# Performance work log

Measured on AMD Instinct MI355X. Metric: run time of the kernel, lower is better.

Reference implementation:

```python
import jax, jax.numpy as jnp
import numpy as np

HID = 128
DEPTH = 3
N_TREE = 6000
N_GRAPH = 144000
N = N_TREE + N_GRAPH
E = 600000
B = 4096
ATOM_FDIM = 34
EPS = 1e-8


def expmap0(u):
    # Lorentz expmap at origin (k=1); u has zero time component u[:,0]=0
    sp = u[:, 1:]
    nrm = jnp.clip(jnp.sqrt(jnp.sum(sp * sp, axis=-1, keepdims=True)), EPS)
    return jnp.concatenate([jnp.cosh(nrm), jnp.sinh(nrm) * sp / nrm], axis=-1)


def lorentz_linear(x, W, b, scale, nonlin=None):
    # HyboNet LorentzLinear: Euclidean linear then reproject onto hyperboloid
    if nonlin is not None:
        x = nonlin(x)
    y = x @ W.T + b
    time = jax.nn.sigmoid(y[:, :1]) * jnp.exp(scale) + 1.1  # [N,1]
    rest = y[:, 1:]
    s = (time * time - 1.0) / jnp.clip(jnp.sum(rest * rest, axis=-1, keepdims=True), EPS)
    return jnp.concatenate([time, rest * jnp.sqrt(s)], axis=-1)


def centroid_denom(x):
    # sqrt(| -<x,x>_L |) = sqrt(| x0^2 - sum(rest^2) |), clamped
    d = x[:, :1] ** 2 - jnp.sum(x[:, 1:] ** 2, axis=-1, keepdims=True)
    return jnp.sqrt(jnp.clip(jnp.abs(d), EPS))


def reference(graph_features, tree_features, edge_w, W0, b0, scale0, Wl, bl, scalel,
              edge_src, edge_dst, seg_ids):
    # prepend zero time coord + expmap0 (Lorentz branch)
    gf = jnp.concatenate([jnp.zeros_like(graph_features[:, :1]), graph_features], axis=1)
    gf = expmap0(gf)
    gf = lorentz_linear(gf, W0, b0, scale0)          # [N_GRAPH, HID]
    x = jnp.concatenate([tree_features, gf], axis=0)  # [N, HID]

    # LorentzGraphConvolution layers: LorentzLinear (relu inside for i>0) + sparse agg
    h = x
    for i in range(DEPTH):
        nonlin = None if i == 0 else jax.nn.relu
        h = lorentz_linear(h, Wl[i], bl[i], scalel[i], nonlin=nonlin)
        msg = edge_w[:, None] * h[edge_src]                         # [E, HID]
        support = jax.ops.segment_sum(msg, edge_dst, num_segments=N)
        h = support / centroid_denom(support)

    # per-scope Lorentz mid-point over graph-atom rows
    hg = h[N_TREE:]
    sums = jax.ops.segment_sum(hg, seg_ids, num_segments=B)
    cnt = jax.ops.segment_sum(jnp.ones((N_GRAPH, 1), h.dtype), seg_ids, num_segments=B)
    ave = sums / jnp.clip(cnt, 1.0)
    mol_vecs = ave / centroid_denom(ave)
    return mol_vecs


def setup_inputs() -> dict:
    key = jax.random.key(0)
    ks = jax.random.split(key, 10)
    log_scale = float(np.log(10.0))
    return {
        'graph_features': jax.random.uniform(ks[0], (N_GRAPH, ATOM_FDIM), jnp.float32),
        'tree_features': jax.random.normal(ks[1], (N_TREE, HID), jnp.float32),
        'edge_w': jax.random.uniform(ks[2], (E,), jnp.float32),
        'W0': jax.random.normal(ks[3], (HID, ATOM_FDIM + 1), jnp.float32) * 0.1,
        'b0': jnp.zeros((HID,), jnp.float32),
        'scale0': jnp.full((1,), log_scale, jnp.float32),
        'Wl': jax.random.normal(ks[4], (DEPTH, HID, HID), jnp.float32) * 0.1,
        'bl': jnp.zeros((DEPTH, HID), jnp.float32),
        'scalel': jnp.full((DEPTH,), log_scale, jnp.float32),
        'edge_src': jax.random.randint(ks[5], (E,), 0, N, jnp.int32),
        'edge_dst': jax.random.randint(ks[6], (E,), 0, N, jnp.int32),
        'seg_ids': jnp.sort(jax.random.randint(ks[7], (N_GRAPH,), 0, B, jnp.int32)),
    }
```

## Files before the change

kernel.cpp:

```cpp
#include <hip/hip_runtime.h>
#include <math.h>

#define HID    128
#define NTREE  6000
#define NGRAPH 144000
#define NNODE  150000
#define NEDGE  600000
#define NSEG   4096
#define AF     34
#define EPSF   1e-8f

#define SCAN_BLK   256
#define SCAN_ELEMS 1024
#define NSCAN ((NNODE + SCAN_ELEMS - 1) / SCAN_ELEMS)


__device__ __forceinline__ float waveReduceSum(float v) {
#pragma unroll
  for (int o = 32; o > 0; o >>= 1) v += __shfl_down(v, o, 64);
  return v;
}

__device__ __forceinline__ float blockReduce128(float v, float* red) {
  v = waveReduceSum(v);
  int w = threadIdx.x >> 6;
  if ((threadIdx.x & 63) == 0) red[w] = v;
  __syncthreads();
  float r = red[0] + red[1];
  __syncthreads();
  return r;
}


__global__ void k_hist(const int* __restrict__ dst, int* __restrict__ deg) {
  int e = blockIdx.x * blockDim.x + threadIdx.x;
  if (e < NEDGE) atomicAdd(&deg[dst[e]], 1);
}

__global__ void k_scan1(const int* __restrict__ deg, int* __restrict__ off,
                        int* __restrict__ part) {
  __shared__ int s[SCAN_BLK];
  int b = blockIdx.x, t = threadIdx.x;
  int base = b * SCAN_ELEMS + t * 4;
  int v0 = 0, v1 = 0, v2 = 0, v3 = 0;
  if (base + 0 < NNODE) v0 = deg[base + 0];
  if (base + 1 < NNODE) v1 = deg[base + 1];
  if (base + 2 < NNODE) v2 = deg[base + 2];
  if (base + 3 < NNODE) v3 = deg[base + 3];
  int sum = v0 + v1 + v2 + v3;
  s[t] = sum;
  __syncthreads();
  for (int o = 1; o < SCAN_BLK; o <<= 1) {
    int x = (t >= o) ? s[t - o] : 0;
    __syncthreads();
    s[t] += x;
    __syncthreads();
  }
  int run = s[t] - sum;
  run += v0; if (base + 0 < NNODE) off[base + 1] = run;
  run += v1; if (base + 1 < NNODE) off[base + 2] = run;
  run += v2; if (base + 2 < NNODE) off[base + 3] = run;
  run += v3; if (base + 3 < NNODE) off[base + 4] = run;
  if (t == SCAN_BLK - 1) part[b] = s[t];
  if (b == 0 && t == 0) off[0] = 0;
}

__global__ void k_scan2(int* part, int nb) {
  __shared__ int s[SCAN_BLK];
  int t = threadIdx.x;
  s[t] = (t < nb) ? part[t] : 0;
  __syncthreads();
  for (int o = 1; o < SCAN_BLK; o <<= 1) {
    int x = (t >= o) ? s[t - o] : 0;
    __syncthreads();
    s[t] += x;
    __syncthreads();
  }
  if (t < nb) part[t] = s[t];
}

__global__ void k_scan3(int* __restrict__ off, const int* __restrict__ part) {
  int b = blockIdx.x;
  if (b == 0) return;
  int add = part[b - 1];
  int base = b * SCAN_ELEMS + threadIdx.x * 4 + 1;
#pragma unroll
  for (int j = 0; j < 4; j++) {
    int idx = base + j;
    if (idx <= NNODE) off[idx] += add;
  }
}

__global__ void k_fill(const int* __restrict__ dst, const int* __restrict__ src,
                       const float* __restrict__ ew, int* __restrict__ cur,
                       int* __restrict__ sperm, float* __restrict__ wperm) {
  int e = blockIdx.x * blockDim.x + threadIdx.x;
  if (e < NEDGE) {
    int d = dst[e];
    int p = atomicAdd(&cur[d], 1);
    sperm[p] = src[e];
    wperm[p] = ew[e];
  }
}


__global__ __launch_bounds__(256) void k_embed(const float* __restrict__ gfeat,
                                               const float* __restrict__ W0,
                                               const float* __restrict__ b0,
                                               const float* __restrict__ scale0,
                                               float* __restrict__ xout) {
  const int lane = threadIdx.x & 63;
  const int gwave = blockIdx.x * (blockDim.x >> 6) + (threadIdx.x >> 6);
  const int nwaves = gridDim.x * (blockDim.x >> 6);

  float wa[AF + 1], wb[AF + 1];
  {
    const float* ra = W0 + (size_t)lane * (AF + 1);
    const float* rb = W0 + (size_t)(lane + 64) * (AF + 1);
#pragma unroll
    for (int k = 0; k < AF + 1; ++k) { wa[k] = ra[k]; wb[k] = rb[k]; }
  }
  const float ba = b0[lane];
  const float bbv = b0[lane + 64];
  const float escale = expf(scale0[0]);

  for (int g = gwave; g < NGRAPH; g += nwaves) {
    float sv = (lane < AF) ? gfeat[(size_t)g * AF + lane] : 0.f;
    float ss = sv * sv;
#pragma unroll
    for (int m = 1; m <= 32; m <<= 1) ss += __shfl_xor(ss, m, 64);
    float nrm = fmaxf(sqrtf(ss), EPSF);
    float e = expf(nrm);
    float ei = 1.f / e;
    float coshv = 0.5f * (e + ei);
    float sh = 0.5f * (e - ei) / nrm;
    float gs = sh * sv;

    float acc0 = fmaf(wa[0], coshv, ba);
    float acc1 = fmaf(wb[0], coshv, bbv);
#pragma unroll
    for (int k = 1; k < AF + 1; ++k) {
      float gk = __int_as_float(
          __builtin_amdgcn_readlane(__float_as_int(gs), k - 1));
      acc0 = fmaf(wa[k], gk, acc0);
      acc1 = fmaf(wb[k], gk, acc1);
    }
    float part = ((lane == 0) ? 0.f : acc0 * acc0) + acc1 * acc1;
#pragma unroll
    for (int m = 1; m <= 32; m <<= 1) part += __shfl_xor(part, m, 64);
    float y0 = __int_as_float(__builtin_amdgcn_readlane(__float_as_int(acc0), 0));
    float timec = 1.f / (1.f + expf(-y0)) * escale + 1.1f;
    float s = (timec * timec - 1.f) / fmaxf(part, EPSF);
    float sq = sqrtf(s);
    float* orow = xout + (size_t)(NTREE + g) * HID;
    orow[lane] = (lane == 0) ? timec : acc0 * sq;
    orow[lane + 64] = acc1 * sq;
  }
}


template <int RELU>
__global__ __launch_bounds__(256) void k_linear(const float* __restrict__ in,
                                                const float* __restrict__ W,
                                                const float* __restrict__ b,
                                                const float* __restrict__ scale,
                                                float* __restrict__ out) {
  __shared__ __align__(16) float xs[32 * 32];
  __shared__ __align__(16) float wl[128 * 32];

  const int tid = threadIdx.x;
  const int tc = tid & 31;
  const int rg = tid >> 5;
  const int c0 = tc * 4;
  const int r0 = rg * 4;
  const int row_base = blockIdx.x * 32;
  const int swz = tc & 7;

  float acc[4][4];
#pragma unroll
  for (int r = 0; r < 4; r++)
#pragma unroll
    for (int c = 0; c < 4; c++) acc[r][c] = 0.f;

  const int sr  = tid >> 3;
  const int skx = (tid & 7) * 4;
  const int wcol = tid >> 1;
  const int wq0  = (tid & 1) * 4;
  const int wswz = (wcol >> 2) & 7;

  for (int kc = 0; kc < 4; ++kc) {
    __syncthreads();
    {
      int row = row_base + sr;
      float4 v = make_float4(0.f, 0.f, 0.f, 0.f);
      if (row < NNODE) v = *(const float4*)&in[(size_t)row * HID + kc * 32 + skx];
      if (RELU) {
        v.x = fmaxf(v.x, 0.f); v.y = fmaxf(v.y, 0.f);
        v.z = fmaxf(v.z, 0.f); v.w = fmaxf(v.w, 0.f);
      }
      *(float4*)&xs[sr * 32 + skx] = v;
    }
    {
      const float* wsrc = W + (size_t)wcol * HID + kc * 32 + wq0 * 4;
#pragma unroll
      for (int q = 0; q < 4; ++q) {
        float4 v = *(const float4*)&wsrc[q * 4];
        int k4 = wq0 + q;
        *(float4*)&wl[wcol * 32 + ((k4 ^ wswz) << 2)] = v;
      }
    }
    __syncthreads();
#pragma unroll
    for (int k4 = 0; k4 < 8; ++k4) {
      float4 xv[4];
      float4 wv[4];
#pragma unroll
      for (int r = 0; r < 4; ++r)
        xv[r] = *(const float4*)&xs[(r0 + r) * 32 + k4 * 4];
#pragma unroll
      for (int c = 0; c < 4; ++c)
        wv[c] = *(const float4*)&wl[(c0 + c) * 32 + ((k4 ^ swz) << 2)];
#pragma unroll
      for (int r = 0; r < 4; ++r)
#pragma unroll
        for (int c = 0; c < 4; ++c)
          acc[r][c] += wv[c].x * xv[r].x + wv[c].y * xv[r].y +
                       wv[c].z * xv[r].z + wv[c].w * xv[r].w;
    }
  }

  const float escale = expf(scale[0]);
  const float4 bb = *(const float4*)&b[c0];
#pragma unroll
  for (int r = 0; r < 4; ++r) {
    float y0v = acc[r][0] + bb.x;
    float y1v = acc[r][1] + bb.y;
    float y2v = acc[r][2] + bb.z;
    float y3v = acc[r][3] + bb.w;
    float part = y0v * y0v + y1v * y1v + y2v * y2v + y3v * y3v;
#pragma unroll
    for (int m = 1; m <= 16; m <<= 1) part += __shfl_xor(part, m, 64);
    float y0 = __shfl(y0v, (threadIdx.x & 32), 64);
    float timec = 1.f / (1.f + expf(-y0)) * escale + 1.1f;
    float ssum = part - y0 * y0;
    float s = (timec * timec - 1.f) / fmaxf(ssum, EPSF);
    float sq = sqrtf(s);
    int row = row_base + r0 + r;
    if (row < NNODE) {
      float4 o;
      o.x = (tc == 0) ? timec : y0v * sq;
      o.y = y1v * sq;
      o.z = y2v * sq;
      o.w = y3v * sq;
      *(float4*)&out[(size_t)row * HID + c0] = o;
    }
  }
}


__global__ void k_gather(const float* __restrict__ h, const int* __restrict__ off,
                         const int* __restrict__ sperm, const float* __restrict__ wperm,
                         float* __restrict__ out) {
  __shared__ float red[2];
  int n = blockIdx.x;
  int t = threadIdx.x;
  int e0 = off[n], e1 = off[n + 1];
  float acc = 0.f;
  for (int e = e0; e < e1; ++e) {
    int s = sperm[e];
    float w = wperm[e];
    acc += w * h[(size_t)s * HID + t];
  }
  float part = (t == 0) ? acc * acc : -acc * acc;
  float d = blockReduce128(part, red);
  float denom = sqrtf(fmaxf(fabsf(d), EPSF));
  out[(size_t)n * HID + t] = acc / denom;
}


__device__ __forceinline__ int lowerBound(const int* __restrict__ a, int n, int key) {
  int lo = 0, hi = n;
  while (lo < hi) {
    int mid = (lo + hi) >> 1;
    if (a[mid] < key) lo = mid + 1; else hi = mid;
  }
  return lo;
}

__global__ void k_final(const float* __restrict__ h, const int* __restrict__ seg,
                        float* __restrict__ out) {
  __shared__ float red[2];
  int bseg = blockIdx.x;
  int t = threadIdx.x;
  int lo = lowerBound(seg, NGRAPH, bseg);
  int hi = lowerBound(seg, NGRAPH, bseg + 1);
  float acc = 0.f;
  for (int r = lo; r < hi; ++r) acc += h[(size_t)(NTREE + r) * HID + t];
  float cnt = (float)(hi - lo);
  float ave = acc / fmaxf(cnt, 1.f);
  float part = (t == 0) ? ave * ave : -ave * ave;
  float d = blockReduce128(part, red);
  float denom = sqrtf(fmaxf(fabsf(d), EPSF));
  out[bseg * HID + t] = ave / denom;
}


extern "C" void kernel_launch(void* const* d_in, const int* in_sizes, int n_in,
                              void* d_out, int out_size, void* d_ws, size_t ws_size,
                              hipStream_t stream) {
  const float* gfeat  = (const float*)d_in[0];
  const float* tfeat  = (const float*)d_in[1];
  const float* ew     = (const float*)d_in[2];
  const float* W0     = (const float*)d_in[3];
  const float* b0     = (const float*)d_in[4];
  const float* scale0 = (const float*)d_in[5];
  const float* Wl     = (const float*)d_in[6];
  const float* bl     = (const float*)d_in[7];
  const float* scalel = (const float*)d_in[8];
  const int* esrc     = (const int*)d_in[9];
  const int* edst     = (const int*)d_in[10];
  const int* segids   = (const int*)d_in[11];
  float* outp = (float*)d_out;

  char* ws = (char*)d_ws;
  size_t o = 0;
  auto take = [&](size_t bytes) -> char* {
    char* p = ws + o;
    o = (o + bytes + 255) & ~(size_t)255;
    return p;
  };
  int*   off   = (int*)take((NNODE + 1) * sizeof(int));
  int*   cur   = (int*)take(NNODE * sizeof(int));
  int*   sperm = (int*)take(NEDGE * sizeof(int));
  float* wperm = (float*)take(NEDGE * sizeof(float));
  int*   part  = (int*)take(SCAN_BLK * sizeof(int));
  float* bufA  = (float*)take((size_t)NNODE * HID * sizeof(float));
  float* bufB  = (float*)take((size_t)NNODE * HID * sizeof(float));
  (void)ws_size; (void)in_sizes; (void)n_in; (void)out_size;

  hipMemsetAsync(cur, 0, NNODE * sizeof(int), stream);
  k_hist<<<(NEDGE + 255) / 256, 256, 0, stream>>>(edst, cur);
  k_scan1<<<NSCAN, SCAN_BLK, 0, stream>>>(cur, off, part);
  k_scan2<<<1, SCAN_BLK, 0, stream>>>(part, NSCAN);
  k_scan3<<<NSCAN, SCAN_BLK, 0, stream>>>(off, part);
  hipMemcpyAsync(cur, off, NNODE * sizeof(int), hipMemcpyDeviceToDevice, stream);
  k_fill<<<(NEDGE + 255) / 256, 256, 0, stream>>>(edst, esrc, ew, cur, sperm, wperm);

  hipMemcpyAsync(bufA, tfeat, (size_t)NTREE * HID * sizeof(float),
                 hipMemcpyDeviceToDevice, stream);
  k_embed<<<1024, 256, 0, stream>>>(gfeat, W0, b0, scale0, bufA);

  for (int i = 0; i < 3; i++) {
    const float* Wi = Wl + (size_t)i * HID * HID;
    const float* bi = bl + (size_t)i * HID;
    const float* si = scalel + i;
    if (i == 0)
      k_linear<0><<<(NNODE + 31) / 32, 256, 0, stream>>>(bufA, Wi, bi, si, bufB);
    else
      k_linear<1><<<(NNODE + 31) / 32, 256, 0, stream>>>(bufA, Wi, bi, si, bufB);
    k_gather<<<NNODE, 128, 0, stream>>>(bufB, off, sperm, wperm, bufA);
  }

  k_final<<<NSEG, 128, 0, stream>>>(bufA, segids, outp);
}
```

Measured before the change: 949.7 us.

## Rewrite k_linear as register-resident weights with one wave per row

Replaces the LDS-tiled 32-row GEMM with a persistent grid-stride kernel. Each lane keeps two full weight rows (256 floats) in registers, and each wave computes one output row with uniform broadcast loads of the input row. This removes shared-memory staging and barriers, but it uses very high register pressure, which lowers occupancy and may cause spills. Each row's input is read as a scalar/uniform broadcast, and arithmetic intensity per wave is lower than with the tiled kernel.

```diff
diff --git a/kernel.cpp b/kernel.cpp
--- a/kernel.cpp
+++ b/kernel.cpp
@@ -165,95 +165,64 @@
                                                 const float* __restrict__ b,
                                                 const float* __restrict__ scale,
                                                 float* __restrict__ out) {
-  __shared__ __align__(16) float xs[32 * 32];
-  __shared__ __align__(16) float wl[128 * 32];
-
-  const int tid = threadIdx.x;
-  const int tc = tid & 31;
-  const int rg = tid >> 5;
-  const int c0 = tc * 4;
-  const int r0 = rg * 4;
-  const int row_base = blockIdx.x * 32;
-  const int swz = tc & 7;
-
-  float acc[4][4];
-#pragma unroll
-  for (int r = 0; r < 4; r++)
-#pragma unroll
-    for (int c = 0; c < 4; c++) acc[r][c] = 0.f;
-
-  const int sr  = tid >> 3;
-  const int skx = (tid & 7) * 4;
-  const int wcol = tid >> 1;
-  const int wq0  = (tid & 1) * 4;
-  const int wswz = (wcol >> 2) & 7;
-
-  for (int kc = 0; kc < 4; ++kc) {
-    __syncthreads();
-    {
-      int row = row_base + sr;
-      float4 v = make_float4(0.f, 0.f, 0.f, 0.f);
-      if (row < NNODE) v = *(const float4*)&in[(size_t)row * HID + kc * 32 + skx];
+  const int lane = threadIdx.x & 63;
+  const int wv = (blockIdx.x * blockDim.x + threadIdx.x) >> 6;
+  const int nw = (gridDim.x * blockDim.x) >> 6;
+
+  float4 wa[32], wb[32];
+  {
+    const float4* ra = (const float4*)(W + (size_t)lane * HID);
+    const float4* rb = (const float4*)(W + (size_t)(lane + 64) * HID);
+#pragma unroll
+    for (int j = 0; j < 32; ++j) { wa[j] = ra[j]; wb[j] = rb[j]; }
+  }
+  const float ba = b[lane];
+  const float bbv = b[lane + 64];
+  const float escale = expf(scale[0]);
+
+  for (int row = wv; row < NNODE; row += nw) {
+    const int urow = __builtin_amdgcn_readfirstlane(row);
+    const float* xr = in + (size_t)urow * HID;
+    float a0 = 0.f, a1 = 0.f, a2 = 0.f, a3 = 0.f;
+#pragma unroll
+    for (int j = 0; j < 32; j += 2) {
+      float4 x0 = *(const float4*)&xr[j * 4];
+      float4 x1 = *(const float4*)&xr[j * 4 + 4];
       if (RELU) {
-        v.x = fmaxf(v.x, 0.f); v.y = fmaxf(v.y, 0.f);
-        v.z = fmaxf(v.z, 0.f); v.w = fmaxf(v.w, 0.f);
+        x0.x = fmaxf(x0.x, 0.f); x0.y = fmaxf(x0.y, 0.f);
+        x0.z = fmaxf(x0.z, 0.f); x0.w = fmaxf(x0.w, 0.f);
+        x1.x = fmaxf(x1.x, 0.f); x1.y = fmaxf(x1.y, 0.f);
+        x1.z = fmaxf(x1.z, 0.f); x1.w = fmaxf(x1.w, 0.f);
       }
-      *(float4*)&xs[sr * 32 + skx] = v;
+      a0 = fmaf(wa[j].x, x0.x, a0);
+      a2 = fmaf(wb[j].x, x0.x, a2);
+      a1 = fmaf(wa[j + 1].x, x1.x, a1);
+      a3 = fmaf(wb[j + 1].x, x1.x, a3);
+      a0 = fmaf(wa[j].y, x0.y, a0);
+      a2 = fmaf(wb[j].y, x0.y, a2);
+      a1 = fmaf(wa[j + 1].y, x1.y, a1);
+      a3 = fmaf(wb[j + 1].y, x1.y, a3);
+      a0 = fmaf(wa[j].z, x0.z, a0);
+      a2 = fmaf(wb[j].z, x0.z, a2);
+      a1 = fmaf(wa[j + 1].z, x1.z, a1);
+      a3 = fmaf(wb[j + 1].z, x1.z, a3);
+      a0 = fmaf(wa[j].w, x0.w, a0);
+      a2 = fmaf(wb[j].w, x0.w, a2);
+      a1 = fmaf(wa[j + 1].w, x1.w, a1);
+      a3 = fmaf(wb[j + 1].w, x1.w, a3);
     }
-    {
-      const float* wsrc = W + (size_t)wcol * HID + kc * 32 + wq0 * 4;
-#pragma unroll
-      for (int q = 0; q < 4; ++q) {
-        float4 v = *(const float4*)&wsrc[q * 4];
-        int k4 = wq0 + q;
-        *(float4*)&wl[wcol * 32 + ((k4 ^ wswz) << 2)] = v;
-      }
-    }
-    __syncthreads();
-#pragma unroll
-    for (int k4 = 0; k4 < 8; ++k4) {
-      float4 xv[4];
-      float4 wv[4];
-#pragma unroll
-      for (int r = 0; r < 4; ++r)
-        xv[r] = *(const float4*)&xs[(r0 + r) * 32 + k4 * 4];
-#pragma unroll
-      for (int c = 0; c < 4; ++c)
-        wv[c] = *(const float4*)&wl[(c0 + c) * 32 + ((k4 ^ swz) << 2)];
-#pragma unroll
-      for (int r = 0; r < 4; ++r)
-#pragma unroll
-        for (int c = 0; c < 4; ++c)
-          acc[r][c] += wv[c].x * xv[r].x + wv[c].y * xv[r].y +
-                       wv[c].z * xv[r].z + wv[c].w * xv[r].w;
-    }
-  }
-
-  const float escale = expf(scale[0]);
-  const float4 bb = *(const float4*)&b[c0];
-#pragma unroll
-  for (int r = 0; r < 4; ++r) {
-    float y0v = acc[r][0] + bb.x;
-    float y1v = acc[r][1] + bb.y;
-    float y2v = acc[r][2] + bb.z;
-    float y3v = acc[r][3] + bb.w;
-    float part = y0v * y0v + y1v * y1v + y2v * y2v + y3v * y3v;
-#pragma unroll
-    for (int m = 1; m <= 16; m <<= 1) part += __shfl_xor(part, m, 64);
-    float y0 = __shfl(y0v, (threadIdx.x & 32), 64);
+    float acc0 = ba + a0 + a1;
+    float acc1 = bbv + a2 + a3;
+    float part = ((lane == 0) ? 0.f : acc0 * acc0) + acc1 * acc1;
+#pragma unroll
+    for (int m = 1; m <= 32; m <<= 1) part += __shfl_xor(part, m, 64);
+    float y0 = __int_as_float(__builtin_amdgcn_readlane(__float_as_int(acc0), 0));
     float timec = 1.f / (1.f + expf(-y0)) * escale + 1.1f;
-    float ssum = part - y0 * y0;
-    float s = (timec * timec - 1.f) / fmaxf(ssum, EPSF);
+    float s = (timec * timec - 1.f) / fmaxf(part, EPSF);
     float sq = sqrtf(s);
-    int row = row_base + r0 + r;
-    if (row < NNODE) {
-      float4 o;
-      o.x = (tc == 0) ? timec : y0v * sq;
-      o.y = y1v * sq;
-      o.z = y2v * sq;
-      o.w = y3v * sq;
-      *(float4*)&out[(size_t)row * HID + c0] = o;
-    }
+    float* orow = out + (size_t)row * HID;
+    orow[lane] = (lane == 0) ? timec : acc0 * sq;
+    orow[lane + 64] = acc1 * sq;
   }
 }
 
@@ -355,9 +324,9 @@
     const float* bi = bl + (size_t)i * HID;
     const float* si = scalel + i;
     if (i == 0)
-      k_linear<0><<<(NNODE + 31) / 32, 256, 0, stream>>>(bufA, Wi, bi, si, bufB);
+      k_linear<0><<<512, 256, 0, stream>>>(bufA, Wi, bi, si, bufB);
     else
-      k_linear<1><<<(NNODE + 31) / 32, 256, 0, stream>>>(bufA, Wi, bi, si, bufB);
+      k_linear<1><<<512, 256, 0, stream>>>(bufA, Wi, bi, si, bufB);
     k_gather<<<NNODE, 128, 0, stream>>>(bufB, off, sperm, wperm, bufA);
   }
 
```

New measurement: 1.902 ms. 100% more time.
